# Performance work log

Measured on AMD Instinct MI355X. Metric: run time of the kernel, lower is better.

## Reference

```python
import jax, jax.numpy as jnp
import numpy as np

N = 400000   # nodes
D = 256      # in_channels
B = 2048     # graphs (segments)
T = 3        # processing steps


def setup_inputs() -> dict:
    key = jax.random.key(0)
    ks = jax.random.split(key, 8)
    s = 0.05
    x = jax.random.normal(ks[0], (N, D), dtype=jnp.float32)
    index = jnp.sort(jax.random.randint(ks[1], (N,), 0, B)).astype(jnp.int64)
    Wih = jax.random.normal(ks[2], (4 * D, 2 * D), dtype=jnp.float32) * s
    Whh = jax.random.normal(ks[3], (4 * D, D), dtype=jnp.float32) * s
    bih = jax.random.normal(ks[4], (4 * D,), dtype=jnp.float32) * s
    bhh = jax.random.normal(ks[5], (4 * D,), dtype=jnp.float32) * s
    Wp = jax.random.normal(ks[6], (D, 2 * D), dtype=jnp.float32) * s
    bp = jax.random.normal(ks[7], (D,), dtype=jnp.float32) * s
    return {"x": x, "index": index, "Wih": Wih, "Whh": Whh,
            "bih": bih, "bhh": bhh, "Wp": Wp, "bp": bp}


def _lstm_step(q_star, h, c, Wih, Whh, bih, bhh):
    # torch LSTM gate order: i, f, g, o
    gates = q_star @ Wih.T + h @ Whh.T + bih + bhh  # [B, 4D]
    i, f, g, o = jnp.split(gates, 4, axis=-1)
    c = jax.nn.sigmoid(f) * c + jax.nn.sigmoid(i) * jnp.tanh(g)
    h = jax.nn.sigmoid(o) * jnp.tanh(c)
    return h, c


def _set2set(x, index, Wih, Whh, bih, bhh):
    h = jnp.zeros((B, D), x.dtype)
    c = jnp.zeros((B, D), x.dtype)
    q_star = jnp.zeros((B, 2 * D), x.dtype)
    for _ in range(T):
        h, c = _lstm_step(q_star, h, c, Wih, Whh, bih, bhh)
        q = h  # [B, D]
        e = jnp.sum(x * q[index], axis=-1)  # [N]
        m = jax.lax.stop_gradient(jax.ops.segment_max(e, index, num_segments=B))
        a = jnp.exp(e - m[index])
        z = jax.ops.segment_sum(a, index, num_segments=B)
        a = a / z[index]                     # segment softmax
        r = jax.ops.segment_sum(a[:, None] * x, index, num_segments=B)  # [B, D]
        q_star = jnp.concatenate([q, r], axis=-1)  # [B, 2D]
    return q_star


def reference(x, index, Wih, Whh, bih, bhh, Wp, bp):
    q_star = _set2set(x, index, Wih, Whh, bih, bhh)
    return q_star @ Wp.T + bp  # [B, D]
```

## Files before the change

kernel.cpp:

```cpp
#include <hip/hip_runtime.h>
#include <hip/hip_bf16.h>
#include <math.h>

#define N_NODES 400000
#define DIM 256
#define NSEG 2048

typedef unsigned short u16;
typedef float floatx4 __attribute__((ext_vector_type(4)));
typedef __bf16 bf16x8 __attribute__((ext_vector_type(8)));

__device__ __forceinline__ u16 f2bf(float f) {
    __hip_bfloat16 h = __float2bfloat16(f);
    return *reinterpret_cast<u16*>(&h);
}
__device__ __forceinline__ float sigf(float x) { return 1.0f / (1.0f + __expf(-x)); }

__global__ void seg_starts_kernel(const int* __restrict__ idx32, int* __restrict__ seg) {
    int n = blockIdx.x * blockDim.x + threadIdx.x;
    if (n >= N_NODES) return;
    const bool is64 = (idx32[N_NODES - 1] == 0);
    int cur  = is64 ? idx32[2 * n] : idx32[n];
    int prev = (n == 0) ? -1 : (is64 ? idx32[2 * (n - 1)] : idx32[n - 1]);
    cur  = min(max(cur, -1), NSEG - 1);
    prev = min(max(prev, -1), NSEG - 1);
    for (int s = prev + 1; s <= cur; ++s) seg[s] = n;
    if (n == N_NODES - 1) {
        for (int s = cur + 1; s <= NSEG; ++s) seg[s] = N_NODES;
    }
}

__global__ void prep_weights_kernel(const float* __restrict__ Wih, const float* __restrict__ Whh,
                                    const float* __restrict__ Wp,
                                    u16* __restrict__ Wc, u16* __restrict__ WpB) {
    int idx = blockIdx.x * blockDim.x + threadIdx.x;
    if (idx < 1024 * 512) {
        int j = idx >> 9, k = idx & 511;
        float v = Wih[(size_t)j * 512 + k];
        if (k < 256) v += Whh[(size_t)j * 256 + k];
        Wc[idx] = f2bf(v);
    }
    if (idx < 256 * 512) WpB[idx] = f2bf(Wp[idx]);
}

__global__ void lstm_bias_kernel(const float* __restrict__ bih, const float* __restrict__ bhh,
                                 float* __restrict__ c, float* __restrict__ h,
                                 u16* __restrict__ A) {
    int idx = blockIdx.x * blockDim.x + threadIdx.x;
    if (idx >= NSEG * DIM) return;
    int b = idx >> 8, d = idx & 255;
    float gi = bih[d]       + bhh[d];
    float gg = bih[d + 512] + bhh[d + 512];
    float go = bih[d + 768] + bhh[d + 768];
    float cn = sigf(gi) * tanhf(gg);
    float hn = sigf(go) * tanhf(cn);
    c[idx] = cn;
    h[idx] = hn;
    A[(size_t)b * 512 + d] = f2bf(hn);
}

__global__ void lstm_pw_kernel(const float* __restrict__ gates,
                               const float* __restrict__ bih, const float* __restrict__ bhh,
                               float* __restrict__ c, float* __restrict__ h,
                               u16* __restrict__ A) {
    int idx = blockIdx.x * blockDim.x + threadIdx.x;
    if (idx >= NSEG * DIM) return;
    int b = idx >> 8, d = idx & 255;
    const float* g = gates + (size_t)b * 1024;
    float gi = g[d]       + bih[d]       + bhh[d];
    float gf = g[d + 256] + bih[d + 256] + bhh[d + 256];
    float gg = g[d + 512] + bih[d + 512] + bhh[d + 512];
    float go = g[d + 768] + bih[d + 768] + bhh[d + 768];
    float cn = sigf(gf) * c[idx] + sigf(gi) * tanhf(gg);
    float hn = sigf(go) * tanhf(cn);
    c[idx] = cn;
    h[idx] = hn;
    A[(size_t)b * 512 + d] = f2bf(hn);
}

__global__ __launch_bounds__(256) void attn_kernel(const float* __restrict__ x,
                                                   const int* __restrict__ seg,
                                                   const float* __restrict__ h,
                                                   u16* __restrict__ A) {
    const int b = blockIdx.x;
    const int tid = threadIdx.x;
    const int wave = tid >> 6, lane = tid & 63;
    int s0 = seg[b], s1 = seg[b + 1];
    s0 = max(s0, 0);
    s1 = min(s1, N_NODES);

    if (s1 <= s0) {
        A[(size_t)b * 512 + 256 + tid] = (u16)0;
        return;
    }

    __shared__ float sm[4], sz[4];
    __shared__ float sr[4][256];

    const float4 qv = *(const float4*)(h + (size_t)b * 256 + lane * 4);

    float m = -INFINITY, z = 0.f;
    float r0 = 0.f, r1 = 0.f, r2 = 0.f, r3 = 0.f;

    for (int n = s0 + wave; n < s1; n += 4) {
        const float4 xv = *(const float4*)(x + (size_t)n * 256 + lane * 4);
        float e = xv.x * qv.x + xv.y * qv.y + xv.z * qv.z + xv.w * qv.w;
        e += __shfl_xor(e, 1);
        e += __shfl_xor(e, 2);
        e += __shfl_xor(e, 4);
        e += __shfl_xor(e, 8);
        e += __shfl_xor(e, 16);
        e += __shfl_xor(e, 32);
        float nm = fmaxf(m, e);
        float corr = __expf(m - nm);
        float p = __expf(e - nm);
        z = z * corr + p;
        r0 = r0 * corr + p * xv.x;
        r1 = r1 * corr + p * xv.y;
        r2 = r2 * corr + p * xv.z;
        r3 = r3 * corr + p * xv.w;
        m = nm;
    }

    if (lane == 0) { sm[wave] = m; sz[wave] = z; }
    sr[wave][lane * 4 + 0] = r0;
    sr[wave][lane * 4 + 1] = r1;
    sr[wave][lane * 4 + 2] = r2;
    sr[wave][lane * 4 + 3] = r3;
    __syncthreads();

    float M = fmaxf(fmaxf(sm[0], sm[1]), fmaxf(sm[2], sm[3]));
    float zz = 0.f, rr = 0.f;
    for (int w = 0; w < 4; ++w) {
        float cw = __expf(sm[w] - M);
        zz += cw * sz[w];
        rr += cw * sr[w][tid];
    }
    A[(size_t)b * 512 + 256 + tid] = f2bf(rr / zz);
}

template<bool BIAS>
__global__ __launch_bounds__(256) void gemm_bt_kernel(const u16* __restrict__ Ag,
                                                      const u16* __restrict__ Wg,
                                                      const float* __restrict__ bias,
                                                      float* __restrict__ C,
                                                      int M, int N, int K) {
    __shared__ __align__(16) u16 As[64][40];
    __shared__ __align__(16) u16 Ws[64][40];

    const int tid = threadIdx.x;
    const int bm = blockIdx.x * 64;
    const int bn = blockIdx.y * 64;
    const int wave = tid >> 6, lane = tid & 63;
    const int wm = (wave & 1) * 32;
    const int wn = (wave >> 1) * 32;
    const int quad = lane >> 4;
    const int r16 = lane & 15;

    const int lrow = tid >> 2;
    const int lcol = (tid & 3) * 8;

    floatx4 acc[2][2] = {};

    for (int k0 = 0; k0 < K; k0 += 32) {
        *(uint4*)&As[lrow][lcol] = *(const uint4*)&Ag[(size_t)(bm + lrow) * K + k0 + lcol];
        *(uint4*)&Ws[lrow][lcol] = *(const uint4*)&Wg[(size_t)(bn + lrow) * K + k0 + lcol];
        __syncthreads();
        bf16x8 af0 = *(const bf16x8*)&As[wm + r16][quad * 8];
        bf16x8 af1 = *(const bf16x8*)&As[wm + 16 + r16][quad * 8];
        bf16x8 wf0 = *(const bf16x8*)&Ws[wn + r16][quad * 8];
        bf16x8 wf1 = *(const bf16x8*)&Ws[wn + 16 + r16][quad * 8];
        acc[0][0] = __builtin_amdgcn_mfma_f32_16x16x32_bf16(af0, wf0, acc[0][0], 0, 0, 0);
        acc[0][1] = __builtin_amdgcn_mfma_f32_16x16x32_bf16(af0, wf1, acc[0][1], 0, 0, 0);
        acc[1][0] = __builtin_amdgcn_mfma_f32_16x16x32_bf16(af1, wf0, acc[1][0], 0, 0, 0);
        acc[1][1] = __builtin_amdgcn_mfma_f32_16x16x32_bf16(af1, wf1, acc[1][1], 0, 0, 0);
        __syncthreads();
    }

    for (int tm = 0; tm < 2; ++tm)
        for (int tn = 0; tn < 2; ++tn)
            for (int j = 0; j < 4; ++j) {
                int row = bm + wm + tm * 16 + quad * 4 + j;
                int col = bn + wn + tn * 16 + r16;
                float v = acc[tm][tn][j];
                if (BIAS) v += bias[col];
                C[(size_t)row * N + col] = v;
            }
}

extern "C" void kernel_launch(void* const* d_in, const int* in_sizes, int n_in,
                              void* d_out, int out_size, void* d_ws, size_t ws_size,
                              hipStream_t stream) {
    const float* x   = (const float*)d_in[0];
    const int*   idx = (const int*)d_in[1];
    const float* Wih = (const float*)d_in[2];
    const float* Whh = (const float*)d_in[3];
    const float* bih = (const float*)d_in[4];
    const float* bhh = (const float*)d_in[5];
    const float* Wp  = (const float*)d_in[6];
    const float* bp  = (const float*)d_in[7];
    float* out = (float*)d_out;

    char* w = (char*)d_ws;
    int*   seg     = (int*)w;    w += 16384;
    u16*   A       = (u16*)w;    w += (size_t)NSEG * 512 * 2;
    u16*   Wc      = (u16*)w;    w += (size_t)1024 * 512 * 2;
    u16*   WpB     = (u16*)w;    w += (size_t)256 * 512 * 2;
    float* h_f32   = (float*)w;  w += (size_t)NSEG * DIM * 4;
    float* c_f32   = (float*)w;  w += (size_t)NSEG * DIM * 4;
    float* gates   = (float*)w;  w += (size_t)NSEG * 1024 * 4;

    seg_starts_kernel<<<(N_NODES + 255) / 256, 256, 0, stream>>>(idx, seg);
    prep_weights_kernel<<<(1024 * 512 + 255) / 256, 256, 0, stream>>>(Wih, Whh, Wp, Wc, WpB);

    lstm_bias_kernel<<<(NSEG * DIM + 255) / 256, 256, 0, stream>>>(bih, bhh, c_f32, h_f32, A);
    attn_kernel<<<NSEG, 256, 0, stream>>>(x, seg, h_f32, A);

    for (int t = 1; t < 3; ++t) {
        gemm_bt_kernel<false><<<dim3(2048 / 64, 1024 / 64), 256, 0, stream>>>(
            A, Wc, nullptr, gates, 2048, 1024, 512);
        lstm_pw_kernel<<<(NSEG * DIM + 255) / 256, 256, 0, stream>>>(gates, bih, bhh,
                                                                     c_f32, h_f32, A);
        attn_kernel<<<NSEG, 256, 0, stream>>>(x, seg, h_f32, A);
    }

    gemm_bt_kernel<true><<<dim3(2048 / 64, 256 / 64), 256, 0, stream>>>(
        A, WpB, bp, out, 2048, 256, 512);
}
```

Before: 762.5 us.

## Cache fp16 copy of x in first attention pass, reuse in later steps

The first attention pass now also writes an fp16 copy of the node features x to workspace. The two later attention passes read this half-size copy instead of the fp32 x, which cuts their memory traffic. They also use half-waves with 8 elements per lane and software-prefetch the next row. The cost is an extra 200MB write in the first pass plus fp16 rounding of x in the later steps.

```diff
diff --git a/kernel.cpp b/kernel.cpp
--- a/kernel.cpp
+++ b/kernel.cpp
@@ -9,6 +9,8 @@
 typedef unsigned short u16;
 typedef float floatx4 __attribute__((ext_vector_type(4)));
 typedef __bf16 bf16x8 __attribute__((ext_vector_type(8)));
+typedef _Float16 f16x4 __attribute__((ext_vector_type(4)));
+typedef _Float16 f16x8 __attribute__((ext_vector_type(8)));
 
 __device__ __forceinline__ u16 f2bf(float f) {
     __hip_bfloat16 h = __float2bfloat16(f);
@@ -78,10 +80,11 @@
     A[(size_t)b * 512 + d] = f2bf(hn);
 }
 
-__global__ __launch_bounds__(256) void attn_kernel(const float* __restrict__ x,
-                                                   const int* __restrict__ seg,
-                                                   const float* __restrict__ h,
-                                                   u16* __restrict__ A) {
+__global__ __launch_bounds__(256) void attn0_kernel(const float* __restrict__ x,
+                                                    const int* __restrict__ seg,
+                                                    const float* __restrict__ h,
+                                                    u16* __restrict__ A,
+                                                    _Float16* __restrict__ xh) {
     const int b = blockIdx.x;
     const int tid = threadIdx.x;
     const int wave = tid >> 6, lane = tid & 63;
@@ -104,6 +107,11 @@
 
     for (int n = s0 + wave; n < s1; n += 4) {
         const float4 xv = *(const float4*)(x + (size_t)n * 256 + lane * 4);
+        f16x4 hv;
+        hv[0] = (_Float16)xv.x; hv[1] = (_Float16)xv.y;
+        hv[2] = (_Float16)xv.z; hv[3] = (_Float16)xv.w;
+        *(f16x4*)(xh + (size_t)n * 256 + lane * 4) = hv;
+
         float e = xv.x * qv.x + xv.y * qv.y + xv.z * qv.z + xv.w * qv.w;
         e += __shfl_xor(e, 1);
         e += __shfl_xor(e, 2);
@@ -139,6 +147,89 @@
     A[(size_t)b * 512 + 256 + tid] = f2bf(rr / zz);
 }
 
+__global__ __launch_bounds__(256) void attn_h_kernel(const _Float16* __restrict__ xh,
+                                                     const int* __restrict__ seg,
+                                                     const float* __restrict__ h,
+                                                     u16* __restrict__ A) {
+    const int b = blockIdx.x;
+    const int tid = threadIdx.x;
+    const int wave = tid >> 6, lane = tid & 63;
+    const int sub = lane >> 5;
+    const int l32 = lane & 31;
+    const int hs = wave * 2 + sub;
+
+    int s0 = seg[b], s1 = seg[b + 1];
+    s0 = max(s0, 0);
+    s1 = min(s1, N_NODES);
+
+    if (s1 <= s0) {
+        A[(size_t)b * 512 + 256 + tid] = (u16)0;
+        return;
+    }
+
+    __shared__ float sm[8], sz[8];
+    __shared__ float sr[8][256];
+
+    float q[8];
+    {
+        const float4 q0 = *(const float4*)(h + (size_t)b * 256 + l32 * 8);
+        const float4 q1 = *(const float4*)(h + (size_t)b * 256 + l32 * 8 + 4);
+        q[0] = q0.x; q[1] = q0.y; q[2] = q0.z; q[3] = q0.w;
+        q[4] = q1.x; q[5] = q1.y; q[6] = q1.z; q[7] = q1.w;
+    }
+
+    float m = -INFINITY, z = 0.f;
+    float r[8] = {};
+
+    int n = s0 + hs;
+    f16x8 cur = {};
+    if (n < s1) cur = *(const f16x8*)(xh + (size_t)n * 256 + l32 * 8);
+
+    while (n < s1) {
+        const int n2 = n + 8;
+        f16x8 nxt = {};
+        if (n2 < s1) nxt = *(const f16x8*)(xh + (size_t)n2 * 256 + l32 * 8);
+
+        float xf[8];
+        float e = 0.f;
+        #pragma unroll
+        for (int j = 0; j < 8; ++j) { xf[j] = (float)cur[j]; e += xf[j] * q[j]; }
+        e += __shfl_xor(e, 1);
+        e += __shfl_xor(e, 2);
+        e += __shfl_xor(e, 4);
+        e += __shfl_xor(e, 8);
+        e += __shfl_xor(e, 16);
+
+        float nm = fmaxf(m, e);
+        float corr = __expf(m - nm);
+        float p = __expf(e - nm);
+        z = z * corr + p;
+        #pragma unroll
+        for (int j = 0; j < 8; ++j) r[j] = r[j] * corr + p * xf[j];
+        m = nm;
+
+        cur = nxt;
+        n = n2;
+    }
+
+    if (l32 == 0) { sm[hs] = m; sz[hs] = z; }
+    #pragma unroll
+    for (int j = 0; j < 8; ++j) sr[hs][l32 * 8 + j] = r[j];
+    __syncthreads();
+
+    float M = sm[0];
+    #pragma unroll
+    for (int w = 1; w < 8; ++w) M = fmaxf(M, sm[w]);
+    float zz = 0.f, rr = 0.f;
+    #pragma unroll
+    for (int w = 0; w < 8; ++w) {
+        float cw = __expf(sm[w] - M);
+        zz += cw * sz[w];
+        rr += cw * sr[w][tid];
+    }
+    A[(size_t)b * 512 + 256 + tid] = f2bf(rr / zz);
+}
+
 template<bool BIAS>
 __global__ __launch_bounds__(256) void gemm_bt_kernel(const u16* __restrict__ Ag,
                                                       const u16* __restrict__ Wg,
@@ -202,26 +293,27 @@
     float* out = (float*)d_out;
 
     char* w = (char*)d_ws;
-    int*   seg     = (int*)w;    w += 16384;
-    u16*   A       = (u16*)w;    w += (size_t)NSEG * 512 * 2;
-    u16*   Wc      = (u16*)w;    w += (size_t)1024 * 512 * 2;
-    u16*   WpB     = (u16*)w;    w += (size_t)256 * 512 * 2;
-    float* h_f32   = (float*)w;  w += (size_t)NSEG * DIM * 4;
-    float* c_f32   = (float*)w;  w += (size_t)NSEG * DIM * 4;
-    float* gates   = (float*)w;  w += (size_t)NSEG * 1024 * 4;
+    int*   seg     = (int*)w;        w += 16384;
+    u16*   A       = (u16*)w;        w += (size_t)NSEG * 512 * 2;
+    u16*   Wc      = (u16*)w;        w += (size_t)1024 * 512 * 2;
+    u16*   WpB     = (u16*)w;        w += (size_t)256 * 512 * 2;
+    float* h_f32   = (float*)w;      w += (size_t)NSEG * DIM * 4;
+    float* c_f32   = (float*)w;      w += (size_t)NSEG * DIM * 4;
+    float* gates   = (float*)w;      w += (size_t)NSEG * 1024 * 4;
+    _Float16* xh   = (_Float16*)w;   w += (size_t)N_NODES * DIM * 2;
 
     seg_starts_kernel<<<(N_NODES + 255) / 256, 256, 0, stream>>>(idx, seg);
     prep_weights_kernel<<<(1024 * 512 + 255) / 256, 256, 0, stream>>>(Wih, Whh, Wp, Wc, WpB);
 
     lstm_bias_kernel<<<(NSEG * DIM + 255) / 256, 256, 0, stream>>>(bih, bhh, c_f32, h_f32, A);
-    attn_kernel<<<NSEG, 256, 0, stream>>>(x, seg, h_f32, A);
+    attn0_kernel<<<NSEG, 256, 0, stream>>>(x, seg, h_f32, A, xh);
 
     for (int t = 1; t < 3; ++t) {
         gemm_bt_kernel<false><<<dim3(2048 / 64, 1024 / 64), 256, 0, stream>>>(
             A, Wc, nullptr, gates, 2048, 1024, 512);
         lstm_pw_kernel<<<(NSEG * DIM + 255) / 256, 256, 0, stream>>>(gates, bih, bhh,
                                                                      c_f32, h_f32, A);
-        attn_kernel<<<NSEG, 256, 0, stream>>>(x, seg, h_f32, A);
+        attn_h_kernel<<<NSEG, 256, 0, stream>>>(xh, seg, h_f32, A);
     }
 
     gemm_bt_kernel<true><<<dim3(2048 / 64, 256 / 64), 256, 0, stream>>>(
```

Result: faster. 711.4 us (-6.7%).
